# Kernel optimization log

Measured on AMD Instinct MI355X. Metric: run time of the kernel, lower is better.

## Reference

```python
import jax, jax.numpy as jnp
import numpy as np

ALPHA = 0.2          # LeakyReLU negative slope
NEG_INF = -9e15      # mask value used by the torch module


def setup_inputs() -> dict:
    key = jax.random.key(0)
    k_x, k_adj, k_w, k_a = jax.random.split(key, 4)
    B, N, D, L = 8, 2048, 128, 3
    x = jax.random.normal(k_x, (B, N, D), dtype=jnp.float32)
    adj = jax.random.randint(k_adj, (B, N, N), 0, 2, dtype=jnp.int32)
    Wg = jax.random.normal(k_w, (L, D, D), dtype=jnp.float32) * 0.08  # ~Linear init scale
    bg = jnp.zeros((L, D), dtype=jnp.float32)
    attn_a = jax.random.normal(k_a, (L, 2 * D), dtype=jnp.float32) * 0.08
    return {"x": x, "adj": adj, "Wg": Wg, "bg": bg, "attn_a": attn_a}


def reference(x, adj, Wg, bg, attn_a):
    # x: [B,N,D], adj: [B,N,N] int, Wg: [L,D,D], bg: [L,D], attn_a: [L,2D]
    D = x.shape[-1]
    L = Wg.shape[0]
    mask = adj > 0
    for i in range(L):  # small fixed layer loop
        h = jax.nn.relu(x @ Wg[i] + bg[i])                       # [B,N,D]
        # a_input[b,i,j] = [h_i, h_j]; dot with a splits into two rank-1 terms,
        # avoiding the N*N*2D intermediate while computing identical math.
        s1 = h @ attn_a[i, :D]                                   # [B,N]
        s2 = h @ attn_a[i, D:]                                   # [B,N]
        e = jax.nn.leaky_relu(s1[:, :, None] + s2[:, None, :], ALPHA)  # [B,N,N]
        e = jnp.where(mask, e, NEG_INF)
        attn = jax.nn.softmax(e, axis=2)                         # masked softmax over neighbors
        # dropout p=0.0 -> identity
        x = x + jnp.einsum('bij,bjd->bid', attn, h)              # residual update
    return x
```

## Files before the change

### kernel.cpp

```cpp
#include <hip/hip_runtime.h>
#include <stdint.h>

typedef __attribute__((ext_vector_type(8))) short short8;
typedef __attribute__((ext_vector_type(4))) float f32x4;
typedef __attribute__((ext_vector_type(16))) float f32x16;
typedef __attribute__((ext_vector_type(4))) unsigned uint4v;

__device__ __forceinline__ unsigned short f2bf(float f) {
    unsigned u = __float_as_uint(f);
    unsigned r = u + 0x7fffu + ((u >> 16) & 1u);
    return (unsigned short)(r >> 16);
}
__device__ __forceinline__ unsigned fenc(float f) {
    unsigned u = __float_as_uint(f);
    return (u & 0x80000000u) ? ~u : (u | 0x80000000u);
}
__device__ __forceinline__ float fdec(unsigned e) {
    unsigned u = (e & 0x80000000u) ? (e & 0x7fffffffu) : ~e;
    return __uint_as_float(u);
}

__global__ __launch_bounds__(256) void k_setup(
    const float* __restrict__ xin, const float* __restrict__ Wf,
    const int* __restrict__ adj, float* __restrict__ xq,
    unsigned short* __restrict__ wTb, unsigned* __restrict__ s2mx,
    unsigned long long* __restrict__ packed)
{
    int blk = blockIdx.x, tid = threadIdx.x;
    if (blk < 2048) {
        int w = (blk * 256 + tid) >> 6;
        int lane = tid & 63;
        for (int k = 0; k < 64; k++) {
            int q = w * 64 + k;
            int row = q >> 5, wd = q & 31;
            int v = adj[row * 2048 + wd * 64 + lane];
            unsigned long long m = __ballot(v > 0);
            if (lane == 0) packed[q] = m;
        }
    } else if (blk < 4096) {
        int e0 = ((blk - 2048) * 256 + tid) * 4;
        *(f32x4*)(xq + e0) = *(const f32x4*)(xin + e0);
    } else if (blk < 4288) {
        int c = (blk - 4096) * 256 + tid;
        int l = c >> 14, rem = c & 16383, n = rem >> 7, k = rem & 127;
        wTb[c] = f2bf(Wf[l * 16384 + k * 128 + n]);
    } else if (tid < 24) {
        s2mx[tid] = fenc(-3e38f);
    }
}

__global__ __launch_bounds__(256) void k_h(
    const float* __restrict__ xq, const unsigned short* __restrict__ wTb,
    const float* __restrict__ bF, const float* __restrict__ aF, int layer,
    unsigned short* __restrict__ hP, float* __restrict__ s1g,
    float* __restrict__ s2g, unsigned* __restrict__ s2mx)
{
    __shared__ short xs[64 * 136];
    __shared__ short wsb[128 * 136];
    __shared__ float s2blk[4];
    int blk = blockIdx.x, tid = threadIdx.x;
    int row0 = blk * 64, b = blk >> 5;
    int w = tid >> 6, lane = tid & 63, quad = lane >> 4, l15 = lane & 15;

    for (int c = tid; c < 1024; c += 256) {
        int r = c >> 4, kg = c & 15;
        const float* src = &xq[(row0 + r) * 128 + kg * 8];
        f32x4 v0 = *(const f32x4*)src;
        f32x4 v1 = *(const f32x4*)(src + 4);
        short8 o;
        o[0] = (short)f2bf(v0[0]); o[1] = (short)f2bf(v0[1]);
        o[2] = (short)f2bf(v0[2]); o[3] = (short)f2bf(v0[3]);
        o[4] = (short)f2bf(v1[0]); o[5] = (short)f2bf(v1[1]);
        o[6] = (short)f2bf(v1[2]); o[7] = (short)f2bf(v1[3]);
        *(short8*)&xs[r * 136 + kg * 8] = o;
    }
    const unsigned short* wl = wTb + layer * 16384;
    for (int c = tid; c < 2048; c += 256) {
        int n = c >> 4, kg = c & 15;
        *(short8*)&wsb[n * 136 + kg * 8] = *(const short8*)&wl[n * 128 + kg * 8];
    }
    __syncthreads();

    f32x4 acc[8];
#pragma unroll
    for (int t = 0; t < 8; t++) acc[t] = {0.f, 0.f, 0.f, 0.f};
#pragma unroll
    for (int ks = 0; ks < 4; ks++) {
        short8 af = *(const short8*)&xs[(w * 16 + l15) * 136 + ks * 32 + quad * 8];
#pragma unroll
        for (int t = 0; t < 8; t++) {
            short8 bf = *(const short8*)&wsb[(t * 16 + l15) * 136 + ks * 32 + quad * 8];
            acc[t] = __builtin_amdgcn_mfma_f32_16x16x32_bf16(af, bf, acc[t], 0, 0, 0);
        }
    }

    float s1p[4] = {0.f, 0.f, 0.f, 0.f}, s2p[4] = {0.f, 0.f, 0.f, 0.f};
#pragma unroll
    for (int t = 0; t < 8; t++) {
        int colg = t * 16 + l15;
        float bgf = bF[layer * 128 + colg];
        float a1 = aF[layer * 256 + colg];
        float a2 = aF[layer * 256 + 128 + colg];
#pragma unroll
        for (int r = 0; r < 4; r++) {
            float v = acc[t][r] + bgf;
            v = v > 0.f ? v : 0.f;
            acc[t][r] = v;
            s1p[r] = fmaf(v, a1, s1p[r]);
            s2p[r] = fmaf(v, a2, s2p[r]);
        }
    }
#pragma unroll
    for (int r = 0; r < 4; r++) {
#pragma unroll
        for (int off = 1; off < 16; off <<= 1) {
            s1p[r] += __shfl_xor(s1p[r], off, 64);
            s2p[r] += __shfl_xor(s2p[r], off, 64);
        }
    }
    if (l15 == 0) {
#pragma unroll
        for (int r = 0; r < 4; r++) {
            int rowg = row0 + w * 16 + quad * 4 + r;
            s1g[rowg] = s1p[r];
            s2g[rowg] = s2p[r];
        }
    }
    float mx = fmaxf(fmaxf(s2p[0], s2p[1]), fmaxf(s2p[2], s2p[3]));
    mx = fmaxf(mx, __shfl_xor(mx, 16, 64));
    mx = fmaxf(mx, __shfl_xor(mx, 32, 64));
    if (lane == 0) s2blk[w] = mx;
    __syncthreads();

    short* st = (short*)wsb;
#pragma unroll
    for (int t = 0; t < 8; t++)
#pragma unroll
        for (int r = 0; r < 4; r++)
            st[(w * 16 + quad * 4 + r) * 130 + t * 16 + l15] = (short)f2bf(acc[t][r]);
    __syncthreads();
    if (tid == 0) {
        float m2 = fmaxf(fmaxf(s2blk[0], s2blk[1]), fmaxf(s2blk[2], s2blk[3]));
        atomicMax(&s2mx[layer * 8 + b], fenc(m2));
    }
    int i0 = (blk & 31) * 64;
    for (int c = tid; c < 1024; c += 256) {
        int t = c >> 8, jl2 = (c >> 6) & 3, sl = c & 63;
        int d = t * 32 + (sl & 31);
        int jloc = jl2 * 16 + (sl >> 5) * 8;
        short8 o;
#pragma unroll
        for (int i = 0; i < 8; i++) o[i] = st[(jloc + i) * 130 + d];
        int jtg = (i0 >> 4) + jl2;
        *(short8*)&hP[(((size_t)(b * 4 + t) * 128 + jtg) * 64 + sl) * 8] = o;
    }
}

__global__ __launch_bounds__(256) void k_attn(
    const unsigned long long* __restrict__ packed,
    const unsigned short* __restrict__ hP, const float* __restrict__ s1g,
    const float* __restrict__ s2g, const unsigned* __restrict__ s2mx,
    int layer, float* __restrict__ xq)
{
    __shared__ float red[3 * 32 * 128];
    __shared__ float red_p[4 * 32];
    int blk = blockIdx.x, tid = threadIdx.x;
    int b = blk >> 6;
    int rowg0 = blk * 32;
    int w = tid >> 6, lane = tid & 63;
    int col = lane & 31, khalf = lane >> 5;

    float s1v = s1g[rowg0 + col];
    float s2m = fdec(s2mx[layer * 8 + b]);
    float tmh = s1v + s2m;
    float mhat = fmaxf(tmh, 0.2f * tmh);

    f32x16 acc[5];
#pragma unroll
    for (int t = 0; t < 5; t++)
#pragma unroll
        for (int r = 0; r < 16; r++) acc[t][r] = 0.f;

    short8 onesf;
    {
        short v = (col == 0) ? (short)0x3F80 : (short)0;
        onesf[0]=v;onesf[1]=v;onesf[2]=v;onesf[3]=v;onesf[4]=v;onesf[5]=v;onesf[6]=v;onesf[7]=v;
    }

    const float* s2b = s2g + b * 2048;
    const unsigned short* hPb = hP + (size_t)b * 4 * 128 * 64 * 8;
    const unsigned long long* prow = packed + (size_t)(rowg0 + col) * 32;

    for (int jl = 0; jl < 32; jl++) {
        int jt = w + jl * 4;
        unsigned long long word = prow[jl];
        unsigned b8 = (unsigned)(word >> (w * 16 + khalf * 8)) & 0xffu;
        int j0 = jt * 16 + khalf * 8;
        f32x4 sa = *(const f32x4*)&s2b[j0];
        f32x4 sb = *(const f32x4*)&s2b[j0 + 4];
        float sv[8] = {sa[0], sa[1], sa[2], sa[3], sb[0], sb[1], sb[2], sb[3]};
        unsigned rp[8];
#pragma unroll
        for (int jj = 0; jj < 8; jj++) {
            float e = s1v + sv[jj];
            e = fmaxf(e, 0.2f * e);
            float pv = __expf(e - mhat);
            rp[jj] = (b8 & (1u << jj)) ? (__float_as_uint(pv) + 0x8000u) : 0u;
        }
        uint4v pk;
        pk[0] = (rp[0] >> 16) | (rp[1] & 0xffff0000u);
        pk[1] = (rp[2] >> 16) | (rp[3] & 0xffff0000u);
        pk[2] = (rp[4] >> 16) | (rp[5] & 0xffff0000u);
        pk[3] = (rp[6] >> 16) | (rp[7] & 0xffff0000u);
        short8 af = *(short8*)&pk;
        short8 bfr[4];
#pragma unroll
        for (int t = 0; t < 4; t++)
            bfr[t] = *(const short8*)&hPb[(((size_t)t * 128 + jt) * 64 + lane) * 8];
#pragma unroll
        for (int t = 0; t < 4; t++)
            acc[t] = __builtin_amdgcn_mfma_f32_32x32x16_bf16(af, bfr[t], acc[t], 0, 0, 0);
        acc[4] = __builtin_amdgcn_mfma_f32_32x32x16_bf16(af, onesf, acc[4], 0, 0, 0);
    }

#pragma unroll
    for (int reg = 0; reg < 16; reg++) {
        int row = (reg & 3) + 8 * (reg >> 2) + 4 * khalf;
        if (w > 0) {
#pragma unroll
            for (int t = 0; t < 4; t++)
                red[(w - 1) * 4096 + row * 128 + t * 32 + col] = acc[t][reg];
        }
        if (col == 0) red_p[w * 32 + row] = acc[4][reg];
    }
    __syncthreads();
    if (w == 0) {
#pragma unroll
        for (int reg = 0; reg < 16; reg++) {
            int row = (reg & 3) + 8 * (reg >> 2) + 4 * khalf;
            float p = red_p[row] + red_p[32 + row] + red_p[64 + row] + red_p[96 + row];
            float rl = p > 0.f ? 1.0f / p : 0.f;
#pragma unroll
            for (int t = 0; t < 4; t++) {
                int cidx = row * 128 + t * 32 + col;
                float o = acc[t][reg] + red[cidx] + red[4096 + cidx] + red[8192 + cidx];
                xq[(rowg0 + row) * 128 + t * 32 + col] += o * rl;
            }
        }
    }
}

extern "C" void kernel_launch(void* const* d_in, const int* in_sizes, int n_in,
                              void* d_out, int out_size, void* d_ws, size_t ws_size,
                              hipStream_t stream) {
    const void* px = d_in[0];
    int ia = 1; long amax = -1;
    for (int i = 1; i < n_in; i++)
        if ((long)in_sizes[i] > amax) { amax = in_sizes[i]; ia = i; }
    int rem[8]; int m = 0;
    for (int i = 1; i < n_in && m < 8; i++) if (i != ia) rem[m++] = i;
    for (int i = 0; i < m; i++)
        for (int j = i + 1; j < m; j++)
            if (in_sizes[rem[j]] > in_sizes[rem[i]]) { int t = rem[i]; rem[i] = rem[j]; rem[j] = t; }
    const int*   padj = (const int*)((n_in > 1) ? d_in[ia] : d_in[0]);
    const float* pW = (const float*)((m > 0) ? d_in[rem[0]] : d_in[0]);
    const float* pa = (const float*)((m > 1) ? d_in[rem[1]] : d_in[0]);
    const float* pb = (const float*)((m > 2) ? d_in[rem[2]] : d_in[0]);

    float* xq = (float*)d_out;
    char* ws = (char*)d_ws;
    unsigned long long* packed = (unsigned long long*)ws;
    unsigned short* hP = (unsigned short*)(ws + 4194304);
    float* s1 = (float*)(ws + 8388608);
    float* s2 = (float*)(ws + 8454144);
    unsigned* s2mx = (unsigned*)(ws + 8519680);
    unsigned short* wTb = (unsigned short*)(ws + 8519808);

    k_setup<<<4289, 256, 0, stream>>>((const float*)px, pW, padj, xq, wTb, s2mx, packed);
    for (int l = 0; l < 3; l++) {
        k_h<<<256, 256, 0, stream>>>(xq, wTb, pb, pa, l, hP, s1, s2, s2mx);
        k_attn<<<512, 256, 0, stream>>>(packed, hP, s1, s2, s2mx, l, xq);
    }
}
```

Baseline: 344.7 us.

## Fuse setup and all layers into one cooperative persistent kernel with grid syncs

Replaces the seven separate launches (setup, then h and attention per layer) with a single cooperative kernel of 256 blocks that uses grid.sync between stages. Each block handles one h tile and two attention row-blocks, sharing one shared-memory buffer. The aim is to remove launch gaps and tail effects between kernels. In exchange, the attention stage now runs on 256 blocks instead of 512, which lowers parallelism, and the setup stage does far more serial work per block. A fallback to the old multi-launch path runs if the cooperative launch fails.

```diff
diff --git a/kernel.cpp b/kernel.cpp
--- a/kernel.cpp
+++ b/kernel.cpp
@@ -1,5 +1,8 @@
 #include <hip/hip_runtime.h>
+#include <hip/hip_cooperative_groups.h>
 #include <stdint.h>
+
+namespace cg = cooperative_groups;
 
 typedef __attribute__((ext_vector_type(8))) short short8;
 typedef __attribute__((ext_vector_type(4))) float f32x4;
@@ -20,45 +23,16 @@
     return __uint_as_float(u);
 }
 
-__global__ __launch_bounds__(256) void k_setup(
-    const float* __restrict__ xin, const float* __restrict__ Wf,
-    const int* __restrict__ adj, float* __restrict__ xq,
-    unsigned short* __restrict__ wTb, unsigned* __restrict__ s2mx,
-    unsigned long long* __restrict__ packed)
-{
-    int blk = blockIdx.x, tid = threadIdx.x;
-    if (blk < 2048) {
-        int w = (blk * 256 + tid) >> 6;
-        int lane = tid & 63;
-        for (int k = 0; k < 64; k++) {
-            int q = w * 64 + k;
-            int row = q >> 5, wd = q & 31;
-            int v = adj[row * 2048 + wd * 64 + lane];
-            unsigned long long m = __ballot(v > 0);
-            if (lane == 0) packed[q] = m;
-        }
-    } else if (blk < 4096) {
-        int e0 = ((blk - 2048) * 256 + tid) * 4;
-        *(f32x4*)(xq + e0) = *(const f32x4*)(xin + e0);
-    } else if (blk < 4288) {
-        int c = (blk - 4096) * 256 + tid;
-        int l = c >> 14, rem = c & 16383, n = rem >> 7, k = rem & 127;
-        wTb[c] = f2bf(Wf[l * 16384 + k * 128 + n]);
-    } else if (tid < 24) {
-        s2mx[tid] = fenc(-3e38f);
-    }
-}
-
-__global__ __launch_bounds__(256) void k_h(
+__device__ __forceinline__ void h_body(
+    int blk, int tid, char* smem, int layer,
     const float* __restrict__ xq, const unsigned short* __restrict__ wTb,
-    const float* __restrict__ bF, const float* __restrict__ aF, int layer,
+    const float* __restrict__ bF, const float* __restrict__ aF,
     unsigned short* __restrict__ hP, float* __restrict__ s1g,
     float* __restrict__ s2g, unsigned* __restrict__ s2mx)
 {
-    __shared__ short xs[64 * 136];
-    __shared__ short wsb[128 * 136];
-    __shared__ float s2blk[4];
-    int blk = blockIdx.x, tid = threadIdx.x;
+    short* xs  = (short*)smem;
+    short* wsb = (short*)(smem + 17408);
+    float* s2blk = (float*)(smem + 52224);
     int row0 = blk * 64, b = blk >> 5;
     int w = tid >> 6, lane = tid & 63, quad = lane >> 4, l15 = lane & 15;
 
@@ -156,17 +130,17 @@
     }
 }
 
-__global__ __launch_bounds__(256) void k_attn(
+__device__ __forceinline__ void attn_body(
+    int rowblk, int tid, char* smem, int layer,
     const unsigned long long* __restrict__ packed,
     const unsigned short* __restrict__ hP, const float* __restrict__ s1g,
     const float* __restrict__ s2g, const unsigned* __restrict__ s2mx,
-    int layer, float* __restrict__ xq)
-{
-    __shared__ float red[3 * 32 * 128];
-    __shared__ float red_p[4 * 32];
-    int blk = blockIdx.x, tid = threadIdx.x;
-    int b = blk >> 6;
-    int rowg0 = blk * 32;
+    float* __restrict__ xq)
+{
+    float* red = (float*)smem;
+    float* red_p = (float*)(smem + 49152);
+    int b = rowblk >> 6;
+    int rowg0 = rowblk * 32;
     int w = tid >> 6, lane = tid & 63;
     int col = lane & 31, khalf = lane >> 5;
 
@@ -184,7 +158,8 @@
     short8 onesf;
     {
         short v = (col == 0) ? (short)0x3F80 : (short)0;
-        onesf[0]=v;onesf[1]=v;onesf[2]=v;onesf[3]=v;onesf[4]=v;onesf[5]=v;onesf[6]=v;onesf[7]=v;
+        onesf[0]=v;onesf[1]=v;onesf[2]=v;onesf[3]=v;
+        onesf[4]=v;onesf[5]=v;onesf[6]=v;onesf[7]=v;
     }
 
     const float* s2b = s2g + b * 2048;
@@ -223,6 +198,7 @@
         acc[4] = __builtin_amdgcn_mfma_f32_32x32x16_bf16(af, onesf, acc[4], 0, 0, 0);
     }
 
+    __syncthreads();
 #pragma unroll
     for (int reg = 0; reg < 16; reg++) {
         int row = (reg & 3) + 8 * (reg >> 2) + 4 * khalf;
@@ -248,12 +224,106 @@
             }
         }
     }
+    __syncthreads();
+}
+
+__global__ __launch_bounds__(256) void k_fused(
+    const float* __restrict__ xin, const float* __restrict__ Wf,
+    const int* __restrict__ adj, const float* __restrict__ bF,
+    const float* __restrict__ aF, float* __restrict__ xq,
+    unsigned short* __restrict__ wTb, unsigned* __restrict__ s2mx,
+    unsigned long long* __restrict__ packed, unsigned short* __restrict__ hP,
+    float* __restrict__ s1g, float* __restrict__ s2g)
+{
+    cg::grid_group grid = cg::this_grid();
+    __shared__ __align__(16) char smem[52304];
+    int blk = blockIdx.x, tid = threadIdx.x;
+    int w = tid >> 6, lane = tid & 63;
+
+    {
+        int qbase = blk * 2048 + w * 512;
+        for (int k = 0; k < 512; k++) {
+            int q = qbase + k;
+            int row = q >> 5, wd = q & 31;
+            int v = adj[row * 2048 + wd * 64 + lane];
+            unsigned long long m = __ballot(v > 0);
+            if (lane == 0) packed[q] = m;
+        }
+        int e0 = blk * 8192 + tid * 32;
+#pragma unroll
+        for (int i = 0; i < 8; i++)
+            *(f32x4*)(xq + e0 + i * 4) = *(const f32x4*)(xin + e0 + i * 4);
+        if (tid < 192) {
+            int c = blk * 192 + tid;
+            int l = c >> 14, rem = c & 16383, n = rem >> 7, kk = rem & 127;
+            wTb[c] = f2bf(Wf[l * 16384 + kk * 128 + n]);
+        }
+        if (blk == 0 && tid < 24) s2mx[tid] = fenc(-3e38f);
+    }
+    grid.sync();
+
+    for (int layer = 0; layer < 3; layer++) {
+        h_body(blk, tid, smem, layer, xq, wTb, bF, aF, hP, s1g, s2g, s2mx);
+        grid.sync();
+        attn_body(blk * 2 + 0, tid, smem, layer, packed, hP, s1g, s2g, s2mx, xq);
+        attn_body(blk * 2 + 1, tid, smem, layer, packed, hP, s1g, s2g, s2mx, xq);
+        grid.sync();
+    }
+}
+
+__global__ __launch_bounds__(256) void k_setup(
+    const float* __restrict__ xin, const float* __restrict__ Wf,
+    const int* __restrict__ adj, float* __restrict__ xq,
+    unsigned short* __restrict__ wTb, unsigned* __restrict__ s2mx,
+    unsigned long long* __restrict__ packed)
+{
+    int blk = blockIdx.x, tid = threadIdx.x;
+    if (blk < 2048) {
+        int w = (blk * 256 + tid) >> 6;
+        int lane = tid & 63;
+        for (int k = 0; k < 64; k++) {
+            int q = w * 64 + k;
+            int row = q >> 5, wd = q & 31;
+            int v = adj[row * 2048 + wd * 64 + lane];
+            unsigned long long m = __ballot(v > 0);
+            if (lane == 0) packed[q] = m;
+        }
+    } else if (blk < 4096) {
+        int e0 = ((blk - 2048) * 256 + tid) * 4;
+        *(f32x4*)(xq + e0) = *(const f32x4*)(xin + e0);
+    } else if (blk < 4288) {
+        int c = (blk - 4096) * 256 + tid;
+        int l = c >> 14, rem = c & 16383, n = rem >> 7, k = rem & 127;
+        wTb[c] = f2bf(Wf[l * 16384 + k * 128 + n]);
+    } else if (tid < 24) {
+        s2mx[tid] = fenc(-3e38f);
+    }
+}
+
+__global__ __launch_bounds__(256) void k_h(
+    const float* __restrict__ xq, const unsigned short* __restrict__ wTb,
+    const float* __restrict__ bF, const float* __restrict__ aF, int layer,
+    unsigned short* __restrict__ hP, float* __restrict__ s1g,
+    float* __restrict__ s2g, unsigned* __restrict__ s2mx)
+{
+    __shared__ __align__(16) char smem[52304];
+    h_body(blockIdx.x, threadIdx.x, smem, layer, xq, wTb, bF, aF, hP, s1g, s2g, s2mx);
+}
+
+__global__ __launch_bounds__(256) void k_attn(
+    const unsigned long long* __restrict__ packed,
+    const unsigned short* __restrict__ hP, const float* __restrict__ s1g,
+    const float* __restrict__ s2g, const unsigned* __restrict__ s2mx,
+    int layer, float* __restrict__ xq)
+{
+    __shared__ __align__(16) char smem[52304];
+    attn_body(blockIdx.x, threadIdx.x, smem, layer, packed, hP, s1g, s2g, s2mx, xq);
 }
 
 extern "C" void kernel_launch(void* const* d_in, const int* in_sizes, int n_in,
                               void* d_out, int out_size, void* d_ws, size_t ws_size,
                               hipStream_t stream) {
-    const void* px = d_in[0];
+    const float* px = (const float*)d_in[0];
     int ia = 1; long amax = -1;
     for (int i = 1; i < n_in; i++)
         if ((long)in_sizes[i] > amax) { amax = in_sizes[i]; ia = i; }
@@ -276,9 +346,18 @@
     unsigned* s2mx = (unsigned*)(ws + 8519680);
     unsigned short* wTb = (unsigned short*)(ws + 8519808);
 
-    k_setup<<<4289, 256, 0, stream>>>((const float*)px, pW, padj, xq, wTb, s2mx, packed);
-    for (int l = 0; l < 3; l++) {
-        k_h<<<256, 256, 0, stream>>>(xq, wTb, pb, pa, l, hP, s1, s2, s2mx);
-        k_attn<<<512, 256, 0, stream>>>(packed, hP, s1, s2, s2mx, l, xq);
-    }
-}
+    void* kargs[] = {
+        (void*)&px, (void*)&pW, (void*)&padj, (void*)&pb, (void*)&pa,
+        (void*)&xq, (void*)&wTb, (void*)&s2mx, (void*)&packed, (void*)&hP,
+        (void*)&s1, (void*)&s2
+    };
+    hipError_t err = hipLaunchCooperativeKernel((void*)k_fused, dim3(256),
+                                                dim3(256), kargs, 0, stream);
+    if (err != hipSuccess) {
+        k_setup<<<4289, 256, 0, stream>>>(px, pW, padj, xq, wTb, s2mx, packed);
+        for (int l = 0; l < 3; l++) {
+            k_h<<<256, 256, 0, stream>>>(xq, wTb, pb, pa, l, hP, s1, s2, s2mx);
+            k_attn<<<512, 256, 0, stream>>>(packed, hP, s1, s2, s2mx, l, xq);
+        }
+    }
+}
```

New measurement: 829.0 us. +140.5%, slower.
